# Kernel tuning notes

Hardware: AMD Instinct MI355X
Metric: run time of the kernel (lower is better)

The kernel has to match this reference:

```python
import jax, jax.numpy as jnp
import numpy as np

DT_RANK = 12


def _mixer(x, in_w, conv_w, conv_b, xproj_w, dt_w, dt_b, A_log, D_skip, out_w):
    # x: [B, L, d_model]
    B, L, _ = x.shape
    d_inner, d_state = A_log.shape
    k = conv_w.shape[-1]
    xz = x @ in_w.T                                  # [B, L, 2*d_inner]
    x_part, z = jnp.split(xz, 2, axis=-1)
    # causal depthwise conv1d (torch pads both sides with k-1 then slices [:L] == left-pad only)
    xc = x_part.transpose(0, 2, 1)                   # [B, d_inner, L]
    xc = jax.lax.conv_general_dilated(
        xc, conv_w, window_strides=(1,), padding=[(k - 1, 0)],
        feature_group_count=d_inner, dimension_numbers=("NCH", "OIH", "NCH"))
    xc = xc + conv_b[None, :, None]
    x_part = jax.nn.silu(xc.transpose(0, 2, 1))      # [B, L, d_inner]
    dt_bc = x_part @ xproj_w.T                       # [B, L, dt_rank + 2*d_state]
    dt_part = dt_bc[..., :DT_RANK]
    b_term = jnp.tanh(dt_bc[..., DT_RANK:DT_RANK + d_state])
    c_term = jnp.tanh(dt_bc[..., DT_RANK + d_state:])
    dt = jax.nn.softplus(dt_part @ dt_w.T + dt_b) + 1e-4   # [B, L, d_inner]
    a = -jnp.exp(A_log)                              # [d_inner, d_state]

    def step(state, inp):
        x_t, dt_t, b_t, c_t = inp                    # [B,di], [B,di], [B,N], [B,N]
        da = jnp.exp(dt_t[:, :, None] * a)           # [B, di, N]
        db = (1.0 - da) * b_t[:, None, :]
        state = da * state + db * x_t[:, :, None]
        y_t = (state * c_t[:, None, :]).sum(-1) + D_skip * x_t
        return state, y_t

    init = jnp.zeros((B, d_inner, d_state), x.dtype)
    xs = (x_part.transpose(1, 0, 2), dt.transpose(1, 0, 2),
          b_term.transpose(1, 0, 2), c_term.transpose(1, 0, 2))
    _, ys = jax.lax.scan(step, init, xs)             # ys: [L, B, d_inner]
    y = ys.transpose(1, 0, 2) * jax.nn.silu(z)
    return y @ out_w.T                               # [B, L, d_model]


def setup_inputs() -> dict:
    key = jax.random.key(0)
    B, L, D = 32, 577, 192
    d_inner, d_state, d_conv = 384, 8, 4
    ks = jax.random.split(key, 16)
    s = 0.02
    inp = {"x": jax.random.normal(ks[0], (B, L, D), jnp.float32)}
    for i, p in enumerate(["fw", "bw"]):
        kk = jax.random.split(ks[1 + i], 8)
        inp[f"{p}_in_w"] = jax.random.normal(kk[0], (2 * d_inner, D), jnp.float32) * s
        inp[f"{p}_conv_w"] = jax.random.normal(kk[1], (d_inner, 1, d_conv), jnp.float32) * 0.1
        inp[f"{p}_conv_b"] = jnp.zeros((d_inner,), jnp.float32)
        inp[f"{p}_xproj_w"] = jax.random.normal(kk[2], (DT_RANK + 2 * d_state, d_inner), jnp.float32) * s
        inp[f"{p}_dt_w"] = jax.random.normal(kk[3], (d_inner, DT_RANK), jnp.float32) * s
        inp[f"{p}_dt_b"] = jnp.zeros((d_inner,), jnp.float32)
        inp[f"{p}_A_log"] = jax.random.uniform(kk[4], (d_inner, d_state), jnp.float32)
        inp[f"{p}_D"] = jnp.ones((d_inner,), jnp.float32)
        inp[f"{p}_out_w"] = jax.random.normal(kk[5], (D, d_inner), jnp.float32) * s
    return inp


def reference(x,
              fw_in_w, fw_conv_w, fw_conv_b, fw_xproj_w, fw_dt_w, fw_dt_b, fw_A_log, fw_D, fw_out_w,
              bw_in_w, bw_conv_w, bw_conv_b, bw_xproj_w, bw_dt_w, bw_dt_b, bw_A_log, bw_D, bw_out_w):
    y_fwd = _mixer(x, fw_in_w, fw_conv_w, fw_conv_b, fw_xproj_w, fw_dt_w, fw_dt_b, fw_A_log, fw_D, fw_out_w)
    x_rev = jnp.flip(x, axis=1)
    y_bwd = _mixer(x_rev, bw_in_w, bw_conv_w, bw_conv_b, bw_xproj_w, bw_dt_w, bw_dt_b, bw_A_log, bw_D, bw_out_w)
    y_bwd = jnp.flip(y_bwd, axis=1)
    return 0.5 * (y_fwd + y_bwd)
```

## Files before the change

kernel.cpp:

```cpp
#include <hip/hip_runtime.h>
#include <hip/hip_bf16.h>

#define L2E 1.44269504088896340f
#define LN2 0.69314718055994531f

typedef __bf16 bf16x8 __attribute__((ext_vector_type(8)));
typedef __bf16 bf16x4 __attribute__((ext_vector_type(4)));
typedef float f32x4 __attribute__((ext_vector_type(4)));

__device__ __forceinline__ float fexp2(float x){ return __builtin_amdgcn_exp2f(x); }
__device__ __forceinline__ float flog2(float x){ return __builtin_amdgcn_logf(x); }
__device__ __forceinline__ float frcp(float x){ return __builtin_amdgcn_rcpf(x); }
__device__ __forceinline__ float fsigmoid(float x){ return frcp(1.f + fexp2(-x*L2E)); }
__device__ __forceinline__ float fsoftplus(float x){
  float sp = flog2(1.f + fexp2(x*L2E))*LN2;
  return (x > 15.f) ? x : sp;
}
__device__ __forceinline__ float ftanh_(float x){
  x = fminf(fmaxf(x, -10.f), 10.f);
  float e = fexp2(2.f*L2E*x);
  return (e - 1.f)*frcp(e + 1.f);
}

#define NB 32
#define LS 577
#define DM 192
#define DI 384
#define BL 18464
#define M2T 36928
#define T_CH 37
#define N_CH 16

__global__ __launch_bounds__(256) void k_prep(
    const float* __restrict__ x,
    const float* __restrict__ fw_in, const float* __restrict__ bw_in,
    const float* __restrict__ fw_out, const float* __restrict__ bw_out,
    const float* __restrict__ fw_xp, const float* __restrict__ bw_xp,
    const float* __restrict__ fw_al, const float* __restrict__ bw_al,
    __hip_bfloat16* __restrict__ xbf, __hip_bfloat16* __restrict__ wcat,
    __hip_bfloat16* __restrict__ wout, __hip_bfloat16* __restrict__ xpp,
    float* __restrict__ alog2)
{
  const int S0 = 3545088;
  const int S1 = S0 + 294912;
  const int S2 = S1 + 147456;
  const int S3 = S2 + 24576;
  const int S4 = S3 + 6144;
  int idx = blockIdx.x*256 + threadIdx.x;
  if (idx < S0) {
    xbf[idx] = __float2bfloat16(x[idx]);
  } else if (idx < S1) {
    int i = idx - S0; int r = i/192, k = i - r*192;
    float v = (r < 768) ? fw_in[r*192+k] : bw_in[(r-768)*192+k];
    wcat[i] = __float2bfloat16(v);
  } else if (idx < S2) {
    int i = idx - S1; int o = i/768, k = i - o*768;
    float v = 0.5f * ((k < 384) ? fw_out[o*384+k] : bw_out[o*384+(k-384)]);
    wout[i] = __float2bfloat16(v);
  } else if (idx < S3) {
    int i = idx - S2; int d = i/12288; int rr = i - d*12288;
    int n = rr/384, k = rr - n*384;
    const float* xp = d ? bw_xp : fw_xp;
    float v = (n < 28) ? xp[n*384+k] : 0.f;
    xpp[i] = __float2bfloat16(v);
  } else if (idx < S4) {
    int i = idx - S3;
    const float* al = (i < 3072) ? fw_al : bw_al;
    int j = (i < 3072) ? i : (i - 3072);
    alog2[i] = -fexp2(al[j]*L2E) * L2E;
  }
}

#define G1_LDA 104
#define G1_LDO 136
__global__ __launch_bounds__(256) void k_gemm1(const __hip_bfloat16* __restrict__ A,
                                               const __hip_bfloat16* __restrict__ Bw,
                                               __hip_bfloat16* __restrict__ xg,
                                               __hip_bfloat16* __restrict__ zsb)
{
  __shared__ __align__(16) __bf16 smem[26624];
  __bf16* ldsA = smem;
  __bf16* ldsB = smem + 128*G1_LDA;

  const int t = threadIdx.x;
  const int tm = blockIdx.x / 12, tn = blockIdx.x - tm*12;
  const int m0 = tm*128, n0 = tn*128;
  const int w = t >> 6, lane = t & 63;
  const int wr = (w >> 1)*64, wc = (w & 1)*64;
  const int r = lane & 15, q = lane >> 4;

  f32x4 acc[4][4];
  #pragma unroll
  for (int a=0;a<4;++a)
    #pragma unroll
    for (int b=0;b<4;++b) acc[a][b] = (f32x4){0.f,0.f,0.f,0.f};

  #pragma unroll
  for (int h=0; h<2; ++h) {
    if (h) __syncthreads();
    #pragma unroll
    for (int j=0;j<6;++j) {
      int cid = t + 256*j;
      int row = cid/12; int c8 = (cid - row*12)*8;
      int gr = m0 + row; if (gr > BL-1) gr = BL-1;
      bf16x8 va = *(const bf16x8*)(A + (size_t)gr*192 + h*96 + c8);
      *(bf16x8*)(ldsA + row*G1_LDA + c8) = va;
      bf16x8 vb = *(const bf16x8*)(Bw + (size_t)(n0+row)*192 + h*96 + c8);
      *(bf16x8*)(ldsB + row*G1_LDA + c8) = vb;
    }
    __syncthreads();
    #pragma unroll
    for (int kc=0; kc<96; kc+=32) {
      bf16x8 af[4], bfv[4];
      #pragma unroll
      for (int mi=0; mi<4; ++mi)
        af[mi] = *(const bf16x8*)(ldsA + (wr + mi*16 + r)*G1_LDA + q*8 + kc);
      #pragma unroll
      for (int ni=0; ni<4; ++ni)
        bfv[ni] = *(const bf16x8*)(ldsB + (wc + ni*16 + r)*G1_LDA + q*8 + kc);
      #pragma unroll
      for (int mi=0; mi<4; ++mi)
        #pragma unroll
        for (int ni=0; ni<4; ++ni)
          acc[mi][ni] = __builtin_amdgcn_mfma_f32_16x16x32_bf16(af[mi], bfv[ni], acc[mi][ni], 0,0,0);
    }
  }

  const int cat = tn/3;
  const int cbase = (tn - cat*3)*128;
  const int d = cat >> 1, isz = cat & 1;
  __syncthreads();
  __bf16* ldsO = smem;
  #pragma unroll
  for (int mi=0; mi<4; ++mi)
    #pragma unroll
    for (int ni=0; ni<4; ++ni)
      #pragma unroll
      for (int rg=0; rg<4; ++rg) {
        int row = wr + mi*16 + q*4 + rg;
        int col = wc + ni*16 + r;
        float v = acc[mi][ni][rg];
        if (isz) v = v * fsigmoid(v);
        ldsO[row*G1_LDO + col] = (__bf16)v;
      }
  __syncthreads();
  __hip_bfloat16* dst = (isz ? zsb : xg) + (size_t)(d*BL)*384 + cbase;
  const int c8 = (t & 15)*8;
  #pragma unroll
  for (int it=0; it<8; ++it) {
    int row = (t >> 4) + it*16;
    int grow = m0 + row;
    if (grow < BL) {
      bf16x8 v = *(const bf16x8*)(ldsO + row*G1_LDO + c8);
      *(bf16x8*)(dst + (size_t)grow*384 + c8) = v;
    }
  }
}

__global__ __launch_bounds__(256) void k_conv(const __hip_bfloat16* __restrict__ xg,
                                              __hip_bfloat16* __restrict__ xcs,
                                              const float* __restrict__ fw_cw, const float* __restrict__ fw_cb,
                                              const float* __restrict__ bw_cw, const float* __restrict__ bw_cb)
{
  int idx = blockIdx.x*256 + threadIdx.x;
  int token = idx / 96; int g = idx - token*96; int c0 = g*4;
  int d = token / BL; int r2 = token - d*BL;
  int b = r2 / LS; int i = r2 - b*LS;
  const float* cwp = (d ? bw_cw : fw_cw);
  const float* cbp = (d ? bw_cb : fw_cb);
  f32x4 w0 = *(const f32x4*)(cwp + (c0+0)*4);
  f32x4 w1 = *(const f32x4*)(cwp + (c0+1)*4);
  f32x4 w2 = *(const f32x4*)(cwp + (c0+2)*4);
  f32x4 w3 = *(const f32x4*)(cwp + (c0+3)*4);
  f32x4 accv = *(const f32x4*)(cbp + c0);
  const __hip_bfloat16* base = xg + ((size_t)(d*BL + b*LS))*384 + c0;
  #pragma unroll
  for (int j=0;j<4;++j) {
    int iw = d ? (i+3-j) : (i-3+j);
    bool valid = d ? (iw < LS) : (iw >= 0);
    if (valid) {
      bf16x4 xv = *(const bf16x4*)(base + (size_t)iw*384);
      f32x4 wj = (f32x4){w0[j], w1[j], w2[j], w3[j]};
      #pragma unroll
      for (int ch=0; ch<4; ++ch) accv[ch] += wj[ch]*(float)xv[ch];
    }
  }
  bf16x4 outv;
  #pragma unroll
  for (int ch=0; ch<4; ++ch) {
    float s = accv[ch]*fsigmoid(accv[ch]);
    outv[ch] = (__bf16)s;
  }
  *(bf16x4*)(xcs + (size_t)token*384 + c0) = outv;
}

__global__ __launch_bounds__(256) void k_dtbc(const __hip_bfloat16* __restrict__ A,
                                              const __hip_bfloat16* __restrict__ xpp,
                                              float* __restrict__ dtbc)
{
  const int wid = blockIdx.x*4 + (threadIdx.x >> 6);
  if (wid >= 1154) return;
  const int lane = threadIdx.x & 63;
  const int m0 = wid*32;
  const int r = lane & 15, q = lane >> 4;
  const int d = (m0 >= BL) ? 1 : 0;
  const __hip_bfloat16* Bp = xpp + (size_t)d*32*384;
  f32x4 acc[2][2];
  #pragma unroll
  for (int a=0;a<2;++a)
    #pragma unroll
    for (int b=0;b<2;++b) acc[a][b] = (f32x4){0.f,0.f,0.f,0.f};
  const __hip_bfloat16* Ab = A + (size_t)(m0 + r)*384 + q*8;
  const __hip_bfloat16* Bb = Bp + (size_t)r*384 + q*8;
  #pragma unroll
  for (int kc = 0; kc < 384; kc += 32) {
    bf16x8 af0 = *(const bf16x8*)(Ab + kc);
    bf16x8 af1 = *(const bf16x8*)(Ab + 16*384 + kc);
    bf16x8 bf0 = *(const bf16x8*)(Bb + kc);
    bf16x8 bf1 = *(const bf16x8*)(Bb + 16*384 + kc);
    acc[0][0] = __builtin_amdgcn_mfma_f32_16x16x32_bf16(af0, bf0, acc[0][0], 0,0,0);
    acc[0][1] = __builtin_amdgcn_mfma_f32_16x16x32_bf16(af0, bf1, acc[0][1], 0,0,0);
    acc[1][0] = __builtin_amdgcn_mfma_f32_16x16x32_bf16(af1, bf0, acc[1][0], 0,0,0);
    acc[1][1] = __builtin_amdgcn_mfma_f32_16x16x32_bf16(af1, bf1, acc[1][1], 0,0,0);
  }
  #pragma unroll
  for (int mi=0; mi<2; ++mi)
    #pragma unroll
    for (int ni=0; ni<2; ++ni)
      #pragma unroll
      for (int rg=0; rg<4; ++rg) {
        int n = ni*16 + r;
        if (n < 28) {
          int m = m0 + mi*16 + q*4 + rg;
          float v = acc[mi][ni][rg];
          if (n >= 12) v = ftanh_(v);
          int r2 = m - d*BL; int b = r2 / LS; int i = r2 - b*LS;
          int ts = d ? (LS-1-i) : i;
          dtbc[((size_t)((d*NB + b)*LS + ts))*28 + n] = v;
        }
      }
}

__global__ __launch_bounds__(64) void k_scan1(const __hip_bfloat16* __restrict__ xcs,
                                              const float* __restrict__ dtbc,
                                              const float* __restrict__ fw_dtw, const float* __restrict__ fw_dtb,
                                              const float* __restrict__ bw_dtw, const float* __restrict__ bw_dtb,
                                              const float* __restrict__ alog2,
                                              float* __restrict__ ps)
{
  __shared__ __align__(16) float sdt[T_CH*28];
  const int bid = blockIdx.x;
  const int lane = threadIdx.x;
  const int kc = bid & 15; const int dbc = bid >> 4;
  const int cchunk = dbc % 6; const int db = dbc / 6;
  const int b = db & 31; const int d = db >> 5;
  const int c = cchunk*64 + lane;

  const int ts0 = kc*T_CH;
  const int ts1 = (ts0 + T_CH < LS) ? (ts0 + T_CH) : LS;

  {
    const float* src = dtbc + ((size_t)((d*NB+b)*LS + ts0))*28;
    int n4 = (ts1 - ts0)*7;
    for (int j = lane; j < n4; j += 64)
      *(f32x4*)(sdt + j*4) = *(const f32x4*)(src + j*4);
  }

  const float* dtwp = (d ? bw_dtw : fw_dtw) + c*12;
  float dtw[12];
  #pragma unroll
  for (int r2=0;r2<12;++r2) dtw[r2] = dtwp[r2];
  const float dtb = (d ? bw_dtb : fw_dtb)[c];
  float al[8];
  const float* alp = alog2 + ((size_t)(d*384 + c))*8;
  #pragma unroll
  for (int s=0;s<8;++s) al[s] = alp[s];

  const __hip_bfloat16* xcb = xcs + ((size_t)(d*BL + b*LS))*384 + c;

  float P[8], S[8];
  #pragma unroll
  for (int s=0;s<8;++s){ P[s]=1.f; S[s]=0.f; }

  __syncthreads();

  float xnb;
  {
    int i = d ? (LS-1-ts0) : ts0;
    xnb = __bfloat162float(xcb[(size_t)i*384]);
  }
  for (int ts=ts0; ts<ts1; ++ts) {
    const float* cur = sdt + (ts-ts0)*28;
    float xt = xnb;
    if (ts+1 < ts1) {
      int i2 = d ? (LS-2-ts) : (ts+1);
      xnb = __bfloat162float(xcb[(size_t)i2*384]);
    }
    float dtr = dtb;
    #pragma unroll
    for (int r2=0;r2<12;++r2) dtr += cur[r2]*dtw[r2];
    float dt = fsoftplus(dtr) + 1e-4f;
    #pragma unroll
    for (int s=0;s<8;++s) {
      float da = fexp2(dt * al[s]);
      float tmp = cur[12+s]*xt;
      S[s] = tmp + da*(S[s]-tmp);
      P[s] *= da;
    }
  }
  float* pp = ps + ((size_t)bid*16)*64 + lane;
  #pragma unroll
  for (int s=0;s<8;++s) pp[s*64] = P[s];
  #pragma unroll
  for (int s=0;s<8;++s) pp[(8+s)*64] = S[s];
}

__global__ __launch_bounds__(64) void k_comb(const float* __restrict__ ps,
                                             float* __restrict__ initst)
{
  const int dbc = blockIdx.x;
  const int lane = threadIdx.x;
  float st[8];
  #pragma unroll
  for (int s=0;s<8;++s) st[s]=0.f;
  for (int kc=0;kc<N_CH;++kc) {
    const float* pp = ps + ((size_t)(dbc*N_CH+kc)*16)*64 + lane;
    float* ip = initst + ((size_t)(dbc*N_CH+kc)*8)*64 + lane;
    #pragma unroll
    for (int s=0;s<8;++s) ip[s*64] = st[s];
    #pragma unroll
    for (int s=0;s<8;++s) {
      float P = pp[s*64], Sv = pp[(8+s)*64];
      st[s] = P*st[s] + Sv;
    }
  }
}

__global__ __launch_bounds__(64) void k_scan2(const __hip_bfloat16* __restrict__ xcs,
                                              const __hip_bfloat16* __restrict__ zsb,
                                              const float* __restrict__ dtbc,
                                              const float* __restrict__ initst,
                                              const float* __restrict__ fw_dtw, const float* __restrict__ fw_dtb,
                                              const float* __restrict__ fw_D,
                                              const float* __restrict__ bw_dtw, const float* __restrict__ bw_dtb,
                                              const float* __restrict__ bw_D,
                                              const float* __restrict__ alog2,
                                              __hip_bfloat16* __restrict__ ybf)
{
  __shared__ __align__(16) float sdt[T_CH*28];
  const int bid = blockIdx.x;
  const int lane = threadIdx.x;
  const int kc = bid & 15; const int dbc = bid >> 4;
  const int cchunk = dbc % 6; const int db = dbc / 6;
  const int b = db & 31; const int d = db >> 5;
  const int c = cchunk*64 + lane;

  const int ts0 = kc*T_CH;
  const int ts1 = (ts0 + T_CH < LS) ? (ts0 + T_CH) : LS;

  {
    const float* src = dtbc + ((size_t)((d*NB+b)*LS + ts0))*28;
    int n4 = (ts1 - ts0)*7;
    for (int j = lane; j < n4; j += 64)
      *(f32x4*)(sdt + j*4) = *(const f32x4*)(src + j*4);
  }

  const float* dtwp = (d ? bw_dtw : fw_dtw) + c*12;
  float dtw[12];
  #pragma unroll
  for (int r2=0;r2<12;++r2) dtw[r2] = dtwp[r2];
  const float dtb = (d ? bw_dtb : fw_dtb)[c];
  const float Dc  = (d ? bw_D : fw_D)[c];
  float al[8];
  const float* alp = alog2 + ((size_t)(d*384 + c))*8;
  #pragma unroll
  for (int s=0;s<8;++s) al[s] = alp[s];

  float st[8];
  {
    const float* ip = initst + ((size_t)bid*8)*64 + lane;
    #pragma unroll
    for (int s=0;s<8;++s) st[s] = ip[s*64];
  }

  const __hip_bfloat16* xcb = xcs + ((size_t)(d*BL + b*LS))*384 + c;
  const __hip_bfloat16* zcb = zsb + ((size_t)(d*BL + b*LS))*384 + c;
  __hip_bfloat16* ybase = ybf + (size_t)(b*LS)*768 + d*384 + c;

  __syncthreads();

  float xnb, znb;
  {
    int i = d ? (LS-1-ts0) : ts0;
    xnb = __bfloat162float(xcb[(size_t)i*384]);
    znb = __bfloat162float(zcb[(size_t)i*384]);
  }
  for (int ts=ts0; ts<ts1; ++ts) {
    const float* cur = sdt + (ts-ts0)*28;
    float xt = xnb, zs = znb;
    int i = d ? (LS-1-ts) : ts;
    if (ts+1 < ts1) {
      int i2 = d ? (LS-2-ts) : (ts+1);
      xnb = __bfloat162float(xcb[(size_t)i2*384]);
      znb = __bfloat162float(zcb[(size_t)i2*384]);
    }
    float dtr = dtb;
    #pragma unroll
    for (int r2=0;r2<12;++r2) dtr += cur[r2]*dtw[r2];
    float dt = fsoftplus(dtr) + 1e-4f;
    float y = Dc * xt;
    #pragma unroll
    for (int s=0;s<8;++s) {
      float da = fexp2(dt * al[s]);
      float tmp = cur[12+s]*xt;
      st[s] = tmp + da*(st[s]-tmp);
      y += st[s]*cur[20+s];
    }
    ybase[(size_t)i*768] = __float2bfloat16(y*zs);
  }
}

__global__ __launch_bounds__(256) void k_gemm2(const __hip_bfloat16* __restrict__ A,
                                               const __hip_bfloat16* __restrict__ Bw,
                                               float* __restrict__ C)
{
  const int wid = blockIdx.x*4 + (threadIdx.x >> 6);
  if (wid >= 1731) return;
  const int lane = threadIdx.x & 63;
  const int tm = wid / 3, tn = wid - tm*3;
  const int m0 = tm*32, n0 = tn*64;
  const int r = lane & 15, q = lane >> 4;
  f32x4 acc[2][4];
  #pragma unroll
  for (int a=0;a<2;++a)
    #pragma unroll
    for (int b=0;b<4;++b) acc[a][b] = (f32x4){0.f,0.f,0.f,0.f};
  const __hip_bfloat16* Ab = A + (size_t)(m0 + r)*768 + q*8;
  const __hip_bfloat16* Bb = Bw + (size_t)(n0 + r)*768 + q*8;
  #pragma unroll 4
  for (int kc = 0; kc < 768; kc += 32) {
    bf16x8 af0 = *(const bf16x8*)(Ab + kc);
    bf16x8 af1 = *(const bf16x8*)(Ab + 16*768 + kc);
    bf16x8 bf0 = *(const bf16x8*)(Bb + kc);
    bf16x8 bf1 = *(const bf16x8*)(Bb + 16*768 + kc);
    bf16x8 bf2 = *(const bf16x8*)(Bb + 32*768 + kc);
    bf16x8 bf3 = *(const bf16x8*)(Bb + 48*768 + kc);
    acc[0][0] = __builtin_amdgcn_mfma_f32_16x16x32_bf16(af0, bf0, acc[0][0], 0,0,0);
    acc[0][1] = __builtin_amdgcn_mfma_f32_16x16x32_bf16(af0, bf1, acc[0][1], 0,0,0);
    acc[0][2] = __builtin_amdgcn_mfma_f32_16x16x32_bf16(af0, bf2, acc[0][2], 0,0,0);
    acc[0][3] = __builtin_amdgcn_mfma_f32_16x16x32_bf16(af0, bf3, acc[0][3], 0,0,0);
    acc[1][0] = __builtin_amdgcn_mfma_f32_16x16x32_bf16(af1, bf0, acc[1][0], 0,0,0);
    acc[1][1] = __builtin_amdgcn_mfma_f32_16x16x32_bf16(af1, bf1, acc[1][1], 0,0,0);
    acc[1][2] = __builtin_amdgcn_mfma_f32_16x16x32_bf16(af1, bf2, acc[1][2], 0,0,0);
    acc[1][3] = __builtin_amdgcn_mfma_f32_16x16x32_bf16(af1, bf3, acc[1][3], 0,0,0);
  }
  #pragma unroll
  for (int mi=0; mi<2; ++mi)
    #pragma unroll
    for (int ni=0; ni<4; ++ni)
      #pragma unroll
      for (int rg=0; rg<4; ++rg) {
        int row = m0 + mi*16 + q*4 + rg;
        int col = n0 + ni*16 + r;
        C[(size_t)row*192 + col] = acc[mi][ni][rg];
      }
}

extern "C" void kernel_launch(void* const* d_in, const int* in_sizes, int n_in,
                              void* d_out, int out_size, void* d_ws, size_t ws_size,
                              hipStream_t stream) {
  const float* x        = (const float*)d_in[0];
  const float* fw_in_w  = (const float*)d_in[1];
  const float* fw_cw    = (const float*)d_in[2];
  const float* fw_cb    = (const float*)d_in[3];
  const float* fw_xp    = (const float*)d_in[4];
  const float* fw_dtw   = (const float*)d_in[5];
  const float* fw_dtb   = (const float*)d_in[6];
  const float* fw_al    = (const float*)d_in[7];
  const float* fw_D     = (const float*)d_in[8];
  const float* fw_ow    = (const float*)d_in[9];
  const float* bw_in_w  = (const float*)d_in[10];
  const float* bw_cw    = (const float*)d_in[11];
  const float* bw_cb    = (const float*)d_in[12];
  const float* bw_xp    = (const float*)d_in[13];
  const float* bw_dtw   = (const float*)d_in[14];
  const float* bw_dtb   = (const float*)d_in[15];
  const float* bw_al    = (const float*)d_in[16];
  const float* bw_D     = (const float*)d_in[17];
  const float* bw_ow    = (const float*)d_in[18];

  char* ws = (char*)d_ws;
  __hip_bfloat16* xbf  = (__hip_bfloat16*)(ws + 0);
  __hip_bfloat16* wcat = (__hip_bfloat16*)(ws + 7090176);
  __hip_bfloat16* wout = (__hip_bfloat16*)(ws + 7680000);
  __hip_bfloat16* xpp  = (__hip_bfloat16*)(ws + 7974912);
  float* alog2         = (float*)(ws + 8024064);
  float* ps            = (float*)(ws + 8048640);
  float* initst        = (float*)(ws + 58380288);
  __hip_bfloat16* ybf  = (__hip_bfloat16*)(ws + 83546112);
  __hip_bfloat16* xg   = (__hip_bfloat16*)(ws + 74158080);
  __hip_bfloat16* xcs  = (__hip_bfloat16*)(ws + 121491456);
  __hip_bfloat16* zsb  = (__hip_bfloat16*)(ws + 149852160);
  float* dtbc          = (float*)(ws + 178212864);

  hipLaunchKernelGGL(k_prep, dim3(15696), dim3(256), 0, stream,
                     x, fw_in_w, bw_in_w, fw_ow, bw_ow, fw_xp, bw_xp, fw_al, bw_al,
                     xbf, wcat, wout, xpp, alog2);
  hipLaunchKernelGGL(k_gemm1, dim3(1740), dim3(256), 0, stream, xbf, wcat, xg, zsb);
  hipLaunchKernelGGL(k_conv, dim3(13848), dim3(256), 0, stream,
                     xg, xcs, fw_cw, fw_cb, bw_cw, bw_cb);
  hipLaunchKernelGGL(k_dtbc, dim3(289), dim3(256), 0, stream, xcs, xpp, dtbc);
  hipLaunchKernelGGL(k_scan1, dim3(6144), dim3(64), 0, stream,
                     xcs, dtbc, fw_dtw, fw_dtb, bw_dtw, bw_dtb, alog2, ps);
  hipLaunchKernelGGL(k_comb, dim3(384), dim3(64), 0, stream, ps, initst);
  hipLaunchKernelGGL(k_scan2, dim3(6144), dim3(64), 0, stream,
                     xcs, zsb, dtbc, initst,
                     fw_dtw, fw_dtb, fw_D, bw_dtw, bw_dtb, bw_D, alog2, ybf);
  hipLaunchKernelGGL(k_gemm2, dim3(433), dim3(256), 0, stream, ybf, wout, (float*)d_out);
}
```

Baseline: 300.4 us.

## Precompute softplus dt in separate kernel instead of recomputing in both scans

```diff
diff --git a/kernel.cpp b/kernel.cpp
--- a/kernel.cpp
+++ b/kernel.cpp
@@ -241,14 +241,29 @@
       }
 }
 
+__global__ __launch_bounds__(256) void k_dtfull(const float* __restrict__ dtbc,
+                                                const float* __restrict__ fw_dtw, const float* __restrict__ fw_dtb,
+                                                const float* __restrict__ bw_dtw, const float* __restrict__ bw_dtb,
+                                                float* __restrict__ dtf)
+{
+  int idx = blockIdx.x*256 + threadIdx.x;
+  int m = idx / 384; int c = idx - m*384;
+  int d = (m >= BL) ? 1 : 0;
+  const float* dtw = (d ? bw_dtw : fw_dtw) + c*12;
+  float dtr = (d ? bw_dtb : fw_dtb)[c];
+  const float* dp = dtbc + (size_t)m*28;
+  #pragma unroll
+  for (int r=0;r<12;++r) dtr += dp[r]*dtw[r];
+  dtf[idx] = fsoftplus(dtr) + 1e-4f;
+}
+
 __global__ __launch_bounds__(64) void k_scan1(const __hip_bfloat16* __restrict__ xcs,
                                               const float* __restrict__ dtbc,
-                                              const float* __restrict__ fw_dtw, const float* __restrict__ fw_dtb,
-                                              const float* __restrict__ bw_dtw, const float* __restrict__ bw_dtb,
+                                              const float* __restrict__ dtf,
                                               const float* __restrict__ alog2,
                                               float* __restrict__ ps)
 {
-  __shared__ __align__(16) float sdt[T_CH*28];
+  __shared__ __align__(16) float sB[T_CH*8];
   const int bid = blockIdx.x;
   const int lane = threadIdx.x;
   const int kc = bid & 15; const int dbc = bid >> 4;
@@ -261,22 +276,18 @@
 
   {
     const float* src = dtbc + ((size_t)((d*NB+b)*LS + ts0))*28;
-    int n4 = (ts1 - ts0)*7;
+    int n4 = (ts1 - ts0)*2;
     for (int j = lane; j < n4; j += 64)
-      *(f32x4*)(sdt + j*4) = *(const f32x4*)(src + j*4);
-  }
-
-  const float* dtwp = (d ? bw_dtw : fw_dtw) + c*12;
-  float dtw[12];
-  #pragma unroll
-  for (int r2=0;r2<12;++r2) dtw[r2] = dtwp[r2];
-  const float dtb = (d ? bw_dtb : fw_dtb)[c];
+      *(f32x4*)(sB + j*4) = *(const f32x4*)(src + (size_t)(j>>1)*28 + 12 + (j&1)*4);
+  }
+
   float al[8];
   const float* alp = alog2 + ((size_t)(d*384 + c))*8;
   #pragma unroll
   for (int s=0;s<8;++s) al[s] = alp[s];
 
   const __hip_bfloat16* xcb = xcs + ((size_t)(d*BL + b*LS))*384 + c;
+  const float* dfb = dtf + ((size_t)((d*NB+b)*LS))*384 + c;
 
   float P[8], S[8];
   #pragma unroll
@@ -284,26 +295,26 @@
 
   __syncthreads();
 
-  float xnb;
+  float xnb, dtn;
   {
     int i = d ? (LS-1-ts0) : ts0;
     xnb = __bfloat162float(xcb[(size_t)i*384]);
+    dtn = dfb[(size_t)ts0*384];
   }
   for (int ts=ts0; ts<ts1; ++ts) {
-    const float* cur = sdt + (ts-ts0)*28;
-    float xt = xnb;
+    f32x4 B0 = *(const f32x4*)(sB + (ts-ts0)*8);
+    f32x4 B1 = *(const f32x4*)(sB + (ts-ts0)*8 + 4);
+    float xt = xnb, dt = dtn;
     if (ts+1 < ts1) {
       int i2 = d ? (LS-2-ts) : (ts+1);
       xnb = __bfloat162float(xcb[(size_t)i2*384]);
-    }
-    float dtr = dtb;
-    #pragma unroll
-    for (int r2=0;r2<12;++r2) dtr += cur[r2]*dtw[r2];
-    float dt = fsoftplus(dtr) + 1e-4f;
+      dtn = dfb[(size_t)(ts+1)*384];
+    }
     #pragma unroll
     for (int s=0;s<8;++s) {
       float da = fexp2(dt * al[s]);
-      float tmp = cur[12+s]*xt;
+      float Bv = (s<4) ? B0[s] : B1[s-4];
+      float tmp = Bv*xt;
       S[s] = tmp + da*(S[s]-tmp);
       P[s] *= da;
     }
@@ -339,15 +350,14 @@
 __global__ __launch_bounds__(64) void k_scan2(const __hip_bfloat16* __restrict__ xcs,
                                               const __hip_bfloat16* __restrict__ zsb,
                                               const float* __restrict__ dtbc,
+                                              const float* __restrict__ dtf,
                                               const float* __restrict__ initst,
-                                              const float* __restrict__ fw_dtw, const float* __restrict__ fw_dtb,
                                               const float* __restrict__ fw_D,
-                                              const float* __restrict__ bw_dtw, const float* __restrict__ bw_dtb,
                                               const float* __restrict__ bw_D,
                                               const float* __restrict__ alog2,
                                               __hip_bfloat16* __restrict__ ybf)
 {
-  __shared__ __align__(16) float sdt[T_CH*28];
+  __shared__ __align__(16) float sBC[T_CH*16];
   const int bid = blockIdx.x;
   const int lane = threadIdx.x;
   const int kc = bid & 15; const int dbc = bid >> 4;
@@ -360,16 +370,11 @@
 
   {
     const float* src = dtbc + ((size_t)((d*NB+b)*LS + ts0))*28;
-    int n4 = (ts1 - ts0)*7;
+    int n4 = (ts1 - ts0)*4;
     for (int j = lane; j < n4; j += 64)
-      *(f32x4*)(sdt + j*4) = *(const f32x4*)(src + j*4);
-  }
-
-  const float* dtwp = (d ? bw_dtw : fw_dtw) + c*12;
-  float dtw[12];
-  #pragma unroll
-  for (int r2=0;r2<12;++r2) dtw[r2] = dtwp[r2];
-  const float dtb = (d ? bw_dtb : fw_dtb)[c];
+      *(f32x4*)(sBC + j*4) = *(const f32x4*)(src + (size_t)(j>>2)*28 + 12 + (j&3)*4);
+  }
+
   const float Dc  = (d ? bw_D : fw_D)[c];
   float al[8];
   const float* alp = alog2 + ((size_t)(d*384 + c))*8;
@@ -385,36 +390,40 @@
 
   const __hip_bfloat16* xcb = xcs + ((size_t)(d*BL + b*LS))*384 + c;
   const __hip_bfloat16* zcb = zsb + ((size_t)(d*BL + b*LS))*384 + c;
+  const float* dfb = dtf + ((size_t)((d*NB+b)*LS))*384 + c;
   __hip_bfloat16* ybase = ybf + (size_t)(b*LS)*768 + d*384 + c;
 
   __syncthreads();
 
-  float xnb, znb;
+  float xnb, znb, dtn;
   {
     int i = d ? (LS-1-ts0) : ts0;
     xnb = __bfloat162float(xcb[(size_t)i*384]);
     znb = __bfloat162float(zcb[(size_t)i*384]);
+    dtn = dfb[(size_t)ts0*384];
   }
   for (int ts=ts0; ts<ts1; ++ts) {
-    const float* cur = sdt + (ts-ts0)*28;
-    float xt = xnb, zs = znb;
+    f32x4 B0 = *(const f32x4*)(sBC + (ts-ts0)*16);
+    f32x4 B1 = *(const f32x4*)(sBC + (ts-ts0)*16 + 4);
+    f32x4 C0 = *(const f32x4*)(sBC + (ts-ts0)*16 + 8);
+    f32x4 C1 = *(const f32x4*)(sBC + (ts-ts0)*16 + 12);
+    float xt = xnb, zs = znb, dt = dtn;
     int i = d ? (LS-1-ts) : ts;
     if (ts+1 < ts1) {
       int i2 = d ? (LS-2-ts) : (ts+1);
       xnb = __bfloat162float(xcb[(size_t)i2*384]);
       znb = __bfloat162float(zcb[(size_t)i2*384]);
-    }
-    float dtr = dtb;
-    #pragma unroll
-    for (int r2=0;r2<12;++r2) dtr += cur[r2]*dtw[r2];
-    float dt = fsoftplus(dtr) + 1e-4f;
+      dtn = dfb[(size_t)(ts+1)*384];
+    }
     float y = Dc * xt;
     #pragma unroll
     for (int s=0;s<8;++s) {
       float da = fexp2(dt * al[s]);
-      float tmp = cur[12+s]*xt;
+      float Bv = (s<4) ? B0[s] : B1[s-4];
+      float Cv = (s<4) ? C0[s] : C1[s-4];
+      float tmp = Bv*xt;
       st[s] = tmp + da*(st[s]-tmp);
-      y += st[s]*cur[20+s];
+      y += st[s]*Cv;
     }
     ybase[(size_t)i*768] = __float2bfloat16(y*zs);
   }
@@ -490,18 +499,19 @@
   const float* bw_ow    = (const float*)d_in[18];
 
   char* ws = (char*)d_ws;
-  __hip_bfloat16* xbf  = (__hip_bfloat16*)(ws + 0);
-  __hip_bfloat16* wcat = (__hip_bfloat16*)(ws + 7090176);
-  __hip_bfloat16* wout = (__hip_bfloat16*)(ws + 7680000);
-  __hip_bfloat16* xpp  = (__hip_bfloat16*)(ws + 7974912);
-  float* alog2         = (float*)(ws + 8024064);
-  float* ps            = (float*)(ws + 8048640);
-  float* initst        = (float*)(ws + 58380288);
-  __hip_bfloat16* ybf  = (__hip_bfloat16*)(ws + 83546112);
-  __hip_bfloat16* xg   = (__hip_bfloat16*)(ws + 74158080);
-  __hip_bfloat16* xcs  = (__hip_bfloat16*)(ws + 121491456);
-  __hip_bfloat16* zsb  = (__hip_bfloat16*)(ws + 149852160);
-  float* dtbc          = (float*)(ws + 178212864);
+  __hip_bfloat16* wcat = (__hip_bfloat16*)(ws + 0);
+  __hip_bfloat16* wout = (__hip_bfloat16*)(ws + 589824);
+  __hip_bfloat16* xpp  = (__hip_bfloat16*)(ws + 884736);
+  float* alog2         = (float*)(ws + 933888);
+  __hip_bfloat16* xbf  = (__hip_bfloat16*)(ws + 958464);
+  __hip_bfloat16* xg   = (__hip_bfloat16*)(ws + 8048640);
+  float* initst        = (float*)(ws + 8048640);
+  __hip_bfloat16* zsb  = (__hip_bfloat16*)(ws + 36409344);
+  __hip_bfloat16* xcs  = (__hip_bfloat16*)(ws + 64770048);
+  float* dtbc          = (float*)(ws + 93130752);
+  float* dtf           = (float*)(ws + 97266688);
+  float* ps            = (float*)(ws + 153988096);
+  __hip_bfloat16* ybf  = (__hip_bfloat16*)(ws + 153988096);
 
   hipLaunchKernelGGL(k_prep, dim3(15696), dim3(256), 0, stream,
                      x, fw_in_w, bw_in_w, fw_ow, bw_ow, fw_xp, bw_xp, fw_al, bw_al,
@@ -510,11 +520,12 @@
   hipLaunchKernelGGL(k_conv, dim3(13848), dim3(256), 0, stream,
                      xg, xcs, fw_cw, fw_cb, bw_cw, bw_cb);
   hipLaunchKernelGGL(k_dtbc, dim3(289), dim3(256), 0, stream, xcs, xpp, dtbc);
+  hipLaunchKernelGGL(k_dtfull, dim3(55392), dim3(256), 0, stream,
+                     dtbc, fw_dtw, fw_dtb, bw_dtw, bw_dtb, dtf);
   hipLaunchKernelGGL(k_scan1, dim3(6144), dim3(64), 0, stream,
-                     xcs, dtbc, fw_dtw, fw_dtb, bw_dtw, bw_dtb, alog2, ps);
+                     xcs, dtbc, dtf, alog2, ps);
   hipLaunchKernelGGL(k_comb, dim3(384), dim3(64), 0, stream, ps, initst);
   hipLaunchKernelGGL(k_scan2, dim3(6144), dim3(64), 0, stream,
-                     xcs, zsb, dtbc, initst,
-                     fw_dtw, fw_dtb, fw_D, bw_dtw, bw_dtb, bw_D, alog2, ybf);
+                     xcs, zsb, dtbc, dtf, initst, fw_D, bw_D, alog2, ybf);
   hipLaunchKernelGGL(k_gemm2, dim3(433), dim3(256), 0, stream, ybf, wout, (float*)d_out);
 }
```

New measurement: 323.9 us. 7.8% more time.
